# Kernel optimization log

Measured on AMD Instinct MI355X. Metric: run time of the kernel, lower is better.

Reference implementation:

```python
import jax, jax.numpy as jnp
import numpy as np

N_NODES = 50000
N_FEAT = 128
N_EDGES = 800000
HEADS1 = 4
HID1 = 64
HID2 = 128
N_CLASSES = 10
N_GRAPHS = 512
NEG_SLOPE_ATT = 0.2   # GATConv attention leaky relu
NEG_SLOPE_ACT = 0.01  # F.leaky_relu default between layers


def setup_inputs() -> dict:
    key = jax.random.key(0)
    ks = jax.random.split(key, 20)
    s = 0.05
    inp = {
        'x': jax.random.normal(ks[0], (N_NODES, N_FEAT), dtype=jnp.float32),
        'edge_index': jax.random.randint(ks[1], (2, N_EDGES), 0, N_NODES, dtype=jnp.int64),
        'edge_attr': jax.random.normal(ks[2], (N_EDGES, 8), dtype=jnp.float32),
        'batch': jnp.sort(jax.random.randint(ks[3], (N_NODES,), 0, N_GRAPHS, dtype=jnp.int64)),
        # conv1: F -> HID1, heads=4, concat
        'W1': jax.random.normal(ks[4], (N_FEAT, HEADS1 * HID1), dtype=jnp.float32) * s,
        'a_src1': jax.random.normal(ks[5], (HEADS1, HID1), dtype=jnp.float32) * s,
        'a_dst1': jax.random.normal(ks[6], (HEADS1, HID1), dtype=jnp.float32) * s,
        'b1': jnp.zeros((HEADS1 * HID1,), dtype=jnp.float32),
        # conv2: 4*HID1 -> HID2, heads=1
        'W2': jax.random.normal(ks[7], (HEADS1 * HID1, HID2), dtype=jnp.float32) * s,
        'a_src2': jax.random.normal(ks[8], (1, HID2), dtype=jnp.float32) * s,
        'a_dst2': jax.random.normal(ks[9], (1, HID2), dtype=jnp.float32) * s,
        'b2': jnp.zeros((HID2,), dtype=jnp.float32),
        # conv3: HID2 -> N_CLASSES, heads=1
        'W3': jax.random.normal(ks[10], (HID2, N_CLASSES), dtype=jnp.float32) * s,
        'a_src3': jax.random.normal(ks[11], (1, N_CLASSES), dtype=jnp.float32) * s,
        'a_dst3': jax.random.normal(ks[12], (1, N_CLASSES), dtype=jnp.float32) * s,
        'b3': jnp.zeros((N_CLASSES,), dtype=jnp.float32),
    }
    return inp


def gat_conv(x, src, dst, W, a_src, a_dst, b, n_nodes, heads, ch):
    """PyG GATConv (concat=True, add_self_loops already applied in src/dst)."""
    h = (x @ W).reshape(n_nodes, heads, ch)            # [N,H,C]
    al_s = (h * a_src).sum(-1)                          # [N,H]
    al_d = (h * a_dst).sum(-1)                          # [N,H]
    e = jax.nn.leaky_relu(al_s[src] + al_d[dst], NEG_SLOPE_ATT)  # [E,H]
    # segment softmax over incoming edges per destination node
    m = jax.ops.segment_max(e, dst, num_segments=n_nodes)
    ex = jnp.exp(e - m[dst])
    den = jax.ops.segment_sum(ex, dst, num_segments=n_nodes)
    alpha = ex / (den[dst] + 1e-16)                     # [E,H]
    out = jax.ops.segment_sum(h[src] * alpha[..., None], dst, num_segments=n_nodes)
    return out.reshape(n_nodes, heads * ch) + b


def reference(x, edge_index, edge_attr, batch,
              W1, a_src1, a_dst1, b1,
              W2, a_src2, a_dst2, b2,
              W3, a_src3, a_dst3, b3):
    # GATConv adds self-loops by default; edge_attr unused (edge_dim=None)
    loops = jnp.arange(N_NODES, dtype=edge_index.dtype)
    src = jnp.concatenate([edge_index[0], loops])
    dst = jnp.concatenate([edge_index[1], loops])

    h = gat_conv(x, src, dst, W1, a_src1, a_dst1, b1, N_NODES, HEADS1, HID1)
    h = jax.nn.leaky_relu(h, NEG_SLOPE_ACT)
    h = gat_conv(h, src, dst, W2, a_src2, a_dst2, b2, N_NODES, 1, HID2)
    h = jax.nn.leaky_relu(h, NEG_SLOPE_ACT)
    h = gat_conv(h, src, dst, W3, a_src3, a_dst3, b3, N_NODES, 1, N_CLASSES)

    pooled = jax.ops.segment_sum(h, batch, num_segments=N_GRAPHS)  # global_add_pool
    return jax.nn.log_softmax(pooled, axis=1), pooled
```

## Files before the change

kernel.cpp:

```cpp
#include <hip/hip_runtime.h>
#include <math.h>

#define NNODES 50000
#define MPAD   50048
#define NFEAT  128
#define NEDGE  800000
#define ETOT   (NEDGE + NNODES)
#define H1     4
#define O1     256
#define C2     128
#define C3     10
#define NGRAPH 512

#define NBKT   196
#define NBLK1  831
#define EPB    1024
#define SCM    (NBKT * NBLK1)
#define SCB    637

typedef __attribute__((ext_vector_type(8))) short short8;
typedef __attribute__((ext_vector_type(4))) float f32x4;
typedef __attribute__((ext_vector_type(2))) float f32x2;

__device__ __forceinline__ unsigned short f2b(float f) {
  unsigned int u = __float_as_uint(f);
  u += 0x7fffu + ((u >> 16) & 1u);
  return (unsigned short)(u >> 16);
}
__device__ __forceinline__ float b2f(unsigned short u) {
  return __uint_as_float(((unsigned int)u) << 16);
}
__device__ __forceinline__ float readlane_f(float v, int l) {
  return __uint_as_float((unsigned)__builtin_amdgcn_readlane(__float_as_uint(v), l));
}


__global__ void k_prep(const float* __restrict__ W1, const float* __restrict__ as1,
                       const float* __restrict__ ad1,
                       float* __restrict__ was, float* __restrict__ wad) {
  int tid = threadIdx.x;
  int h = tid >> 7, k = tid & 127;
  float s = 0.f, d = 0.f;
  for (int j = 0; j < 64; ++j) {
    float w = W1[(size_t)k * 256 + h * 64 + j];
    s += w * as1[h * 64 + j];
    d += w * ad1[h * 64 + j];
  }
  was[h * 128 + k] = s;
  wad[h * 128 + k] = d;
}

#define NB_CVT 12500

__global__ __launch_bounds__(256) void k_front(
    const int* __restrict__ src_e, const int* __restrict__ dst_e,
    int* __restrict__ hists,
    const float* __restrict__ X, unsigned short* __restrict__ Xb,
    const float* __restrict__ W1,
    const float* __restrict__ was, const float* __restrict__ wad,
    float* __restrict__ als, float* __restrict__ ald,
    unsigned short* __restrict__ W1p,
    const float* __restrict__ W2, unsigned short* __restrict__ W2p,
    const float* __restrict__ W3, unsigned short* __restrict__ W3p) {
  const int b = blockIdx.x;
  const int tid = threadIdx.x;
  if (b < NBLK1) {
    __shared__ int h[NBKT];
    if (tid < NBKT) h[tid] = 0;
    __syncthreads();
    const int base = b * EPB;
#pragma unroll
    for (int r = 0; r < 4; ++r) {
      int e = base + r * 256 + tid;
      if (e < ETOT) {
        int d = (e < NEDGE) ? dst_e[e] : (e - NEDGE);
        atomicAdd(&h[d >> 8], 1);
      }
    }
    __syncthreads();
    if (tid < NBKT) hists[tid * NBLK1 + b] = h[tid];
  } else if (b < NBLK1 + NB_CVT) {
    const int n = (b - NBLK1) * 4 + (tid >> 6);
    const int lane = tid & 63;
    const int k0 = lane * 2;
    float2 xv = *(const float2*)(X + (size_t)n * 128 + k0);
    ushort2 o; o.x = f2b(xv.x); o.y = f2b(xv.y);
    *(ushort2*)(Xb + (size_t)n * 128 + k0) = o;
    float s[4], d[4];
#pragma unroll
    for (int h = 0; h < 4; ++h) {
      float2 wsv = *(const float2*)(was + h * 128 + k0);
      float2 wdv = *(const float2*)(wad + h * 128 + k0);
      s[h] = xv.x * wsv.x + xv.y * wsv.y;
      d[h] = xv.x * wdv.x + xv.y * wdv.y;
    }
#pragma unroll
    for (int m = 1; m < 64; m <<= 1)
#pragma unroll
      for (int h = 0; h < 4; ++h) { s[h] += __shfl_xor(s[h], m); d[h] += __shfl_xor(d[h], m); }
    if (lane == 0) {
#pragma unroll
      for (int h = 0; h < 4; ++h) {
        als[(size_t)n * 4 + h] = s[h];
        ald[(size_t)n * 4 + h] = d[h];
      }
    }
  } else if (b < NBLK1 + NB_CVT + 128) {
    int idx = (b - NBLK1 - NB_CVT) * 256 + tid;
    int h = idx >> 13, r = idx & 8191;
    int j = r & 7, lane = (r >> 3) & 63, t = r >> 9;
    int ks = t & 3, nt = t >> 2;
    int k = ks * 32 + (lane >> 4) * 8 + j;
    int n = nt * 16 + (lane & 15);
    W1p[idx] = f2b(W1[(size_t)k * 256 + h * 64 + n]);
  } else if (b < NBLK1 + NB_CVT + 256) {
    int idx = (b - NBLK1 - NB_CVT - 128) * 256 + tid;
    int j = idx & 7, lane = (idx >> 3) & 63, t = idx >> 9;
    int ks = t % 8, nt = t / 8;
    int k = ks * 32 + (lane >> 4) * 8 + j;
    int n = nt * 16 + (lane & 15);
    W2p[idx] = f2b(W2[(size_t)k * C2 + n]);
  } else {
    int idx = (b - NBLK1 - NB_CVT - 256) * 256 + tid;
    int j = idx & 7, lane = (idx >> 3) & 63, t = idx >> 9;
    int ks = t & 3, nt = t >> 2;
    int k = ks * 32 + (lane >> 4) * 8 + j;
    int n = nt * 16 + (lane & 15);
    W3p[idx] = f2b((n < C3) ? W3[(size_t)k * C3 + n] : 0.f);
  }
}


__global__ __launch_bounds__(256) void k_scanA2(const int* __restrict__ a,
                                                int* __restrict__ bsum) {
  int idx = blockIdx.x * 256 + threadIdx.x;
  int v = (idx < SCM) ? a[idx] : 0;
#pragma unroll
  for (int m = 1; m < 64; m <<= 1) v += __shfl_xor(v, m);
  __shared__ int ws[4];
  int lane = threadIdx.x & 63, wid = threadIdx.x >> 6;
  if (lane == 0) ws[wid] = v;
  __syncthreads();
  if (threadIdx.x == 0) bsum[blockIdx.x] = ws[0] + ws[1] + ws[2] + ws[3];
}

__global__ __launch_bounds__(256) void k_scanMid(int* __restrict__ bsum) {
  __shared__ int ws[4];
  __shared__ int carry_s;
  const int tid = threadIdx.x, lane = tid & 63, wid = tid >> 6;
  if (tid == 0) carry_s = 0;
  __syncthreads();
  for (int base = 0; base < SCB; base += 256) {
    int j = base + tid;
    int v = (j < SCB) ? bsum[j] : 0;
    int s = v;
#pragma unroll
    for (int m = 1; m < 64; m <<= 1) {
      int t = __shfl_up(s, m);
      if (lane >= m) s += t;
    }
    if (lane == 63) ws[wid] = s;
    __syncthreads();
    int woff = 0;
#pragma unroll
    for (int k = 0; k < 4; ++k)
      if (k < wid) woff += ws[k];
    int c = carry_s;
    int tot = ws[0] + ws[1] + ws[2] + ws[3];
    if (j < SCB) bsum[j] = c + woff + s - v;
    __syncthreads();
    if (tid == 0) carry_s = c + tot;
    __syncthreads();
  }
}

__global__ __launch_bounds__(256) void k_scanB2(int* __restrict__ a,
                                                const int* __restrict__ bsum,
                                                int* __restrict__ cb) {
  const int b = blockIdx.x, tid = threadIdx.x;
  const int lane = tid & 63, wid = tid >> 6;
  __shared__ int ws[4];
  int idx = b * 256 + tid;
  int v = (idx < SCM) ? a[idx] : 0;
  int s = v;
#pragma unroll
  for (int m = 1; m < 64; m <<= 1) {
    int t = __shfl_up(s, m);
    if (lane >= m) s += t;
  }
  if (lane == 63) ws[wid] = s;
  __syncthreads();
  int woff = 0;
#pragma unroll
  for (int k = 0; k < 4; ++k)
    if (k < wid) woff += ws[k];
  int excl = bsum[b] + woff + s - v;
  if (idx < SCM) {
    a[idx] = excl;
    if (idx % NBLK1 == 0) cb[idx / NBLK1] = excl;
  }
  if (b == 0 && tid == 0) cb[NBKT] = ETOT;
}


__global__ __launch_bounds__(256) void k_part1(const int* __restrict__ src_e,
                                               const int* __restrict__ dst_e,
                                               const int* __restrict__ offs,
                                               unsigned* __restrict__ coarse) {
  __shared__ int cur[NBKT];
  const int b = blockIdx.x;
  const int tid = threadIdx.x;
  if (tid < NBKT) cur[tid] = offs[tid * NBLK1 + b];
  __syncthreads();
  const int base = b * EPB;
#pragma unroll
  for (int r = 0; r < 4; ++r) {
    int e = base + r * 256 + tid;
    if (e < ETOT) {
      int d, s;
      if (e < NEDGE) { d = dst_e[e]; s = src_e[e]; }
      else           { d = e - NEDGE; s = e - NEDGE; }
      int pos = atomicAdd(&cur[d >> 8], 1);
      coarse[pos] = ((unsigned)d << 16) | (unsigned)s;
    }
  }
}


__global__ __launch_bounds__(256) void k_bucket(const unsigned* __restrict__ coarse,
                                                const int* __restrict__ cb,
                                                int* __restrict__ rowptr,
                                                int* __restrict__ srcs) {
  const int b = blockIdx.x;
  const int tid = threadIdx.x;
  const int lane = tid & 63, wid = tid >> 6;
  const int lo = cb[b], hi = cb[b + 1];
  __shared__ int h[256];
  __shared__ int cur[256];
  __shared__ int ws[4];
  h[tid] = 0;
  __syncthreads();
  for (int i = lo + tid; i < hi; i += 256)
    atomicAdd(&h[(coarse[i] >> 16) & 255], 1);
  __syncthreads();
  int v = h[tid];
  int s = v;
#pragma unroll
  for (int m = 1; m < 64; m <<= 1) {
    int t = __shfl_up(s, m);
    if (lane >= m) s += t;
  }
  if (lane == 63) ws[wid] = s;
  __syncthreads();
  int woff = 0;
#pragma unroll
  for (int k = 0; k < 4; ++k)
    if (k < wid) woff += ws[k];
  int ex = woff + s - v;
  cur[tid] = lo + ex;
  int d = b * 256 + tid;
  if (d < NNODES) rowptr[d] = lo + ex;
  if (b == NBKT - 1 && tid == 0) rowptr[NNODES] = ETOT;
  __syncthreads();
  for (int i = lo + tid; i < hi; i += 256) {
    unsigned c = coarse[i];
    int pos = atomicAdd(&cur[(c >> 16) & 255], 1);
    srcs[pos] = (int)(c & 0xffffu);
  }
}


__global__ __launch_bounds__(512) void k_aggP(const int* __restrict__ rowptr,
                                              const int* __restrict__ srcs,
                                              const unsigned short* __restrict__ Xb,
                                              const float* __restrict__ als,
                                              const float* __restrict__ ald,
                                              unsigned short* __restrict__ P) {
  __shared__ float exs[8][16][4];
  const int wv = threadIdx.x >> 6;
  const int n = blockIdx.x * 8 + wv;
  const int lane = threadIdx.x & 63;
  const int r0 = rowptr[n], r1 = rowptr[n + 1];
  const int e_lane = lane & 15, hh = lane >> 4;
  const float aldv = ald[(size_t)n * 4 + hh];
  const int ch0 = lane * 2;
  f32x2 ah0 = {0.f, 0.f}, ah1 = {0.f, 0.f}, ah2 = {0.f, 0.f}, ah3 = {0.f, 0.f};
  float den = 0.f;
  for (int i0 = r0; i0 < r1; i0 += 16) {
    const int take = r1 - i0;
    int sidx = srcs[min(i0 + e_lane, r1 - 1)];
    float ev = als[(size_t)sidx * 4 + hh] + aldv;
    ev = (ev > 0.f) ? ev : 0.2f * ev;
    float exv = (e_lane < take) ? __expf(ev) : 0.f;
    den += exv;
    exs[wv][e_lane][hh] = exv;
    unsigned hv[16];
#pragma unroll
    for (int m = 0; m < 16; ++m) {
      int s = __builtin_amdgcn_readlane(sidx, m);
      hv[m] = *(const unsigned*)(Xb + (size_t)s * 128 + ch0);
    }
#pragma unroll
    for (int m = 0; m < 16; ++m) {
      f32x2 e01 = *(const f32x2*)(&exs[wv][m][0]);
      f32x2 e23 = *(const f32x2*)(&exs[wv][m][2]);
      f32x2 x2;
      x2.x = __uint_as_float(hv[m] << 16);
      x2.y = __uint_as_float(hv[m] & 0xffff0000u);
      asm("v_pk_fma_f32 %0, %1, %2, %0 op_sel:[0,0,0] op_sel_hi:[1,0,1]"
          : "+v"(ah0) : "v"(x2), "v"(e01));
      asm("v_pk_fma_f32 %0, %1, %2, %0 op_sel:[0,1,0] op_sel_hi:[1,1,1]"
          : "+v"(ah1) : "v"(x2), "v"(e01));
      asm("v_pk_fma_f32 %0, %1, %2, %0 op_sel:[0,0,0] op_sel_hi:[1,0,1]"
          : "+v"(ah2) : "v"(x2), "v"(e23));
      asm("v_pk_fma_f32 %0, %1, %2, %0 op_sel:[0,1,0] op_sel_hi:[1,1,1]"
          : "+v"(ah3) : "v"(x2), "v"(e23));
    }
  }
#pragma unroll
  for (int m = 1; m < 16; m <<= 1) den += __shfl_xor(den, m);
  float acc[4][2] = {{ah0.x, ah0.y}, {ah1.x, ah1.y}, {ah2.x, ah2.y}, {ah3.x, ah3.y}};
#pragma unroll
  for (int h = 0; h < 4; ++h) {
    float rd = 1.f / (readlane_f(den, h * 16) + 1e-16f);
    ushort2 o; o.x = f2b(acc[h][0] * rd); o.y = f2b(acc[h][1] * rd);
    *(ushort2*)(P + ((size_t)n * 4 + h) * 128 + ch0) = o;
  }
}


__global__ __launch_bounds__(256) void k_mmX(
    const unsigned short* __restrict__ P,
    const unsigned short* __restrict__ W1p, const float* __restrict__ b1,
    const unsigned short* __restrict__ W2p,
    const float* __restrict__ as2, const float* __restrict__ ad2,
    unsigned short* __restrict__ Hout,
    float* __restrict__ als, float* __restrict__ ald) {
  __shared__ unsigned short actl[64 * 256];
  const int wv = threadIdx.x >> 6, lane = threadIdx.x & 63;
  const int row16 = lane & 15;
  const int k0 = (lane >> 4) * 8;
  const int col = lane & 15;
  const int rb = (lane >> 4) * 4;

  const int nodebase = blockIdx.x * 64 + wv * 16;
#pragma unroll
  for (int h = 0; h < 4; ++h) {
    const unsigned short* Ph = P + ((size_t)(nodebase + row16) * 4 + h) * 128;
    f32x4 acc[4] = {};
#pragma unroll
    for (int ks = 0; ks < 4; ++ks) {
      short8 a = *(const short8*)(Ph + ks * 32 + k0);
      const short8* bp = (const short8*)(W1p + (size_t)h * 8192) + ks * 64 + lane;
#pragma unroll
      for (int nt = 0; nt < 4; ++nt) {
        short8 b = bp[nt * 256];
        acc[nt] = __builtin_amdgcn_mfma_f32_16x16x32_bf16(a, b, acc[nt], 0, 0, 0);
      }
    }
#pragma unroll
    for (int nt = 0; nt < 4; ++nt) {
      int ch = h * 64 + nt * 16 + col;
      float bb = b1[ch];
#pragma unroll
      for (int j = 0; j < 4; ++j) {
        int row = wv * 16 + rb + j;
        float v = acc[nt][j] + bb;
        v = (v > 0.f) ? v : 0.01f * v;
        unsigned byte = (unsigned)(row * 512 + ch * 2) ^ (unsigned)((row & 7) << 4);
        *(unsigned short*)((char*)actl + byte) = f2b(v);
      }
    }
  }
  __syncthreads();

  const int arow = wv * 16 + row16;
  f32x4 acc2[8] = {};
#pragma unroll
  for (int ks = 0; ks < 8; ++ks) {
    unsigned byte = (unsigned)(arow * 512 + (ks * 32 + k0) * 2) ^
                    (unsigned)((arow & 7) << 4);
    short8 a = *(const short8*)((const char*)actl + byte);
    const short8* bp = (const short8*)W2p + ks * 64 + lane;
#pragma unroll
    for (int nt = 0; nt < 8; ++nt) {
      short8 b = bp[(size_t)nt * 512];
      acc2[nt] = __builtin_amdgcn_mfma_f32_16x16x32_bf16(a, b, acc2[nt], 0, 0, 0);
    }
  }
  const int rbase = blockIdx.x * 64 + wv * 16 + rb;
  float av[8], dv[8];
#pragma unroll
  for (int nt = 0; nt < 8; ++nt) {
    int ch = nt * 16 + col;
    av[nt] = as2[ch];
    dv[nt] = ad2[ch];
#pragma unroll
    for (int j = 0; j < 4; ++j)
      Hout[(size_t)(rbase + j) * C2 + ch] = f2b(acc2[nt][j]);
  }
  float sa[4] = {0.f, 0.f, 0.f, 0.f}, da[4] = {0.f, 0.f, 0.f, 0.f};
#pragma unroll
  for (int nt = 0; nt < 8; ++nt)
#pragma unroll
    for (int j = 0; j < 4; ++j) {
      sa[j] += acc2[nt][j] * av[nt];
      da[j] += acc2[nt][j] * dv[nt];
    }
#pragma unroll
  for (int mask = 1; mask < 16; mask <<= 1)
#pragma unroll
    for (int j = 0; j < 4; ++j) {
      sa[j] += __shfl_xor(sa[j], mask);
      da[j] += __shfl_xor(da[j], mask);
    }
  if (col == 0) {
#pragma unroll
    for (int j = 0; j < 4; ++j) {
      als[rbase + j] = sa[j];
      ald[rbase + j] = da[j];
    }
  }
}


__global__ __launch_bounds__(512) void k_agg2(const int* __restrict__ rowptr,
                                              const int* __restrict__ srcs,
                                              const unsigned short* __restrict__ Hm,
                                              const float* __restrict__ als,
                                              const float* __restrict__ ald,
                                              const float* __restrict__ bias,
                                              const unsigned short* __restrict__ W3p,
                                              const float* __restrict__ as3,
                                              const float* __restrict__ ad3,
                                              unsigned short* __restrict__ H3b,
                                              float* __restrict__ als3,
                                              float* __restrict__ ald3) {
  __shared__ float exs2[8][16];
  __shared__ unsigned short Xl[8][128];
  const int wv = threadIdx.x >> 6;
  const int n = blockIdx.x * 8 + wv;
  const int lane = threadIdx.x & 63;
  const int r0 = rowptr[n], r1 = rowptr[n + 1];
  const int e_lane = lane & 15;
  const int ch0 = lane * 2;
  const float aldm = ald[n];
  f32x2 accP0 = {0.f, 0.f}, accP1 = {0.f, 0.f};
  float den = 0.f;
  for (int i0 = r0; i0 < r1; i0 += 16) {
    const int take = r1 - i0;
    int sidx = srcs[min(i0 + e_lane, r1 - 1)];
    float ev = als[sidx] + aldm;
    ev = (ev > 0.f) ? ev : 0.2f * ev;
    float exv = (lane < 16 && e_lane < take) ? __expf(ev) : 0.f;
    den += exv;
    if (lane < 16) exs2[wv][lane] = exv;
    unsigned hv[16];
#pragma unroll
    for (int m = 0; m < 16; ++m) {
      int s = __builtin_amdgcn_readlane(sidx, m);
      hv[m] = *(const unsigned*)(Hm + (size_t)s * C2 + ch0);
    }
#pragma unroll
    for (int m = 0; m < 16; m += 2) {
      f32x2 ep = *(const f32x2*)(&exs2[wv][m]);
      f32x2 xa, xb;
      xa.x = __uint_as_float(hv[m] << 16);
      xa.y = __uint_as_float(hv[m + 1] << 16);
      xb.x = __uint_as_float(hv[m] & 0xffff0000u);
      xb.y = __uint_as_float(hv[m + 1] & 0xffff0000u);
      asm("v_pk_fma_f32 %0, %1, %2, %0" : "+v"(accP0) : "v"(ep), "v"(xa));
      asm("v_pk_fma_f32 %0, %1, %2, %0" : "+v"(accP1) : "v"(ep), "v"(xb));
    }
  }
#pragma unroll
  for (int mask = 1; mask < 64; mask <<= 1) den += __shfl_xor(den, mask);
  float rden = 1.f / (den + 1e-16f);
  float v0 = (accP0.x + accP0.y) * rden + bias[ch0];
  float v1 = (accP1.x + accP1.y) * rden + bias[ch0 + 1];
  v0 = (v0 > 0.f) ? v0 : 0.01f * v0;
  v1 = (v1 > 0.f) ? v1 : 0.01f * v1;
  ushort2 o; o.x = f2b(v0); o.y = f2b(v1);
  *(ushort2*)(&Xl[wv][ch0]) = o;
  __syncthreads();

  if (wv == 0) {
    const int row = lane & 15;
    const int k0 = (lane >> 4) * 8;
    const int col = lane & 15;
    f32x4 acc2 = {};
#pragma unroll
    for (int ks = 0; ks < 4; ++ks) {
      short8 a{};
      if (row < 8) a = *(const short8*)(&Xl[row][ks * 32 + k0]);
      short8 b = *((const short8*)W3p + ks * 64 + lane);
      acc2 = __builtin_amdgcn_mfma_f32_16x16x32_bf16(a, b, acc2, 0, 0, 0);
    }
    const float av = (col < C3) ? as3[col] : 0.f;
    const float dv = (col < C3) ? ad3[col] : 0.f;
    const int rb = (lane >> 4) * 4;
#pragma unroll
    for (int j = 0; j < 4; ++j) {
      float hv = acc2[j];
      float sa = hv * av, da = hv * dv;
#pragma unroll
      for (int mask = 1; mask < 16; mask <<= 1) {
        sa += __shfl_xor(sa, mask);
        da += __shfl_xor(da, mask);
      }
      int r = rb + j;
      if (r < 8) {
        int node = blockIdx.x * 8 + r;
        H3b[(size_t)node * 16 + col] = f2b(hv);
        if (col == 0) { als3[node] = sa; ald3[node] = da; }
      }
    }
  }
}


__global__ __launch_bounds__(512) void k_agg3(const int* __restrict__ rowptr,
                                              const int* __restrict__ srcs,
                                              const unsigned short* __restrict__ Hm,
                                              const float* __restrict__ als,
                                              const float* __restrict__ ald,
                                              const float* __restrict__ bias,
                                              float* __restrict__ pooled,
                                              const int* __restrict__ batch) {
  __shared__ int   sid_s[8][4][16];
  __shared__ float exv_s[8][4][16];
  const int wv = threadIdx.x >> 6;
  const int lane = threadIdx.x & 63;
  const int g = lane >> 4, el = lane & 15;
  const int n = blockIdx.x * 32 + wv * 4 + g;
  const bool valid = n < NNODES;
  int r0 = 0, r1 = 0;
  float aldm = 0.f;
  if (valid) { r0 = rowptr[n]; r1 = rowptr[n + 1]; aldm = ald[n]; }
  float acc = 0.f, den = 0.f;
  for (int i0 = r0; i0 < r1; i0 += 16) {
    const int take = r1 - i0;
    int sidx = srcs[min(i0 + el, r1 - 1)];
    float ev = als[sidx] + aldm;
    ev = (ev > 0.f) ? ev : 0.2f * ev;
    float exv = (el < take) ? __expf(ev) : 0.f;
    den += exv;
    sid_s[wv][g][el] = sidx;
    exv_s[wv][g][el] = exv;
#pragma unroll
    for (int m = 0; m < 16; ++m) {
      int s = sid_s[wv][g][m];
      float ex = exv_s[wv][g][m];
      acc += ex * b2f(Hm[(size_t)s * 16 + el]);
    }
  }
#pragma unroll
  for (int mask = 1; mask < 16; mask <<= 1) den += __shfl_xor(den, mask);
  if (valid && el < C3) {
    float val = acc / (den + 1e-16f) + bias[el];
    atomicAdd(&pooled[(size_t)batch[n] * C3 + el], val);
  }
}


__global__ void k_lsm(const float* __restrict__ pooled, float* __restrict__ dout) {
  int g = blockIdx.x * 256 + threadIdx.x;
  if (g >= NGRAPH) return;
  float v[C3];
  float mx = -1e30f;
#pragma unroll
  for (int c = 0; c < C3; ++c) { v[c] = pooled[g * C3 + c]; mx = fmaxf(mx, v[c]); }
  float ssum = 0.f;
#pragma unroll
  for (int c = 0; c < C3; ++c) ssum += __expf(v[c] - mx);
  float lse = mx + __logf(ssum);
#pragma unroll
  for (int c = 0; c < C3; ++c) {
    dout[g * C3 + c] = v[c] - lse;
    dout[NGRAPH * C3 + g * C3 + c] = v[c];
  }
}


extern "C" void kernel_launch(void* const* d_in, const int* in_sizes, int n_in,
                              void* d_out, int out_size, void* d_ws, size_t ws_size,
                              hipStream_t stream) {
  (void)in_sizes; (void)n_in; (void)out_size; (void)ws_size;
  const float* x     = (const float*)d_in[0];
  const int*   eix   = (const int*)d_in[1];
  const int*   batch = (const int*)d_in[3];
  const float* W1 = (const float*)d_in[4];
  const float* as1 = (const float*)d_in[5];
  const float* ad1 = (const float*)d_in[6];
  const float* b1 = (const float*)d_in[7];
  const float* W2 = (const float*)d_in[8];
  const float* as2 = (const float*)d_in[9];
  const float* ad2 = (const float*)d_in[10];
  const float* b2 = (const float*)d_in[11];
  const float* W3 = (const float*)d_in[12];
  const float* as3 = (const float*)d_in[13];
  const float* ad3 = (const float*)d_in[14];
  const float* b3 = (const float*)d_in[15];
  const int* src_e = eix;
  const int* dst_e = eix + NEDGE;

  char* ws = (char*)d_ws;
  size_t off = 0;
  auto carve = [&](size_t bytes) -> char* {
    char* p = ws + off;
    off += (bytes + 511) & ~(size_t)511;
    return p;
  };
  int* hists  = (int*)carve((size_t)SCM * 4);
  int* bsum   = (int*)carve((size_t)SCB * 4);
  int* cb     = (int*)carve((size_t)(NBKT + 1) * 4);
  unsigned* coarse = (unsigned*)carve((size_t)ETOT * 4);
  int* rowptr = (int*)carve((size_t)(NNODES + 1) * 4);
  int* srcs   = (int*)carve((size_t)ETOT * 4);
  float* als  = (float*)carve((size_t)MPAD * H1 * 4);
  float* ald  = (float*)carve((size_t)MPAD * H1 * 4);
  float* als3 = (float*)carve((size_t)MPAD * 4);
  float* ald3 = (float*)carve((size_t)MPAD * 4);
  float* was  = (float*)carve((size_t)512 * 4);
  float* wad  = (float*)carve((size_t)512 * 4);
  unsigned short* Xb  = (unsigned short*)carve((size_t)MPAD * 128 * 2);
  unsigned short* P   = (unsigned short*)carve((size_t)MPAD * 512 * 2);
  unsigned short* Hb  = (unsigned short*)carve((size_t)MPAD * 128 * 2);
  unsigned short* H3b = (unsigned short*)carve((size_t)MPAD * 16 * 2);
  float* pooled = (float*)carve((size_t)NGRAPH * C3 * 4);
  unsigned short* W1p = (unsigned short*)carve((size_t)4 * 8192 * 2);
  unsigned short* W2p = (unsigned short*)carve((size_t)O1 * C2 * 2);
  unsigned short* W3p = (unsigned short*)carve((size_t)C2 * 16 * 2);

  hipMemsetAsync(pooled, 0, (size_t)NGRAPH * C3 * 4, stream);

  k_prep<<<1, 512, 0, stream>>>(W1, as1, ad1, was, wad);
  k_front<<<NBLK1 + NB_CVT + 264, 256, 0, stream>>>(
      src_e, dst_e, hists, x, Xb, W1, was, wad, als, ald, W1p, W2, W2p, W3, W3p);
  k_scanA2<<<SCB, 256, 0, stream>>>(hists, bsum);
  k_scanMid<<<1, 256, 0, stream>>>(bsum);
  k_scanB2<<<SCB, 256, 0, stream>>>(hists, bsum, cb);
  k_part1<<<NBLK1, 256, 0, stream>>>(src_e, dst_e, hists, coarse);
  k_bucket<<<NBKT, 256, 0, stream>>>(coarse, cb, rowptr, srcs);

  const int GB = MPAD / 64;
  const int NB8 = NNODES / 8;
  const int NB32 = (NNODES + 31) / 32;

  k_aggP<<<NB8, 512, 0, stream>>>(rowptr, srcs, Xb, als, ald, P);
  k_mmX<<<GB, 256, 0, stream>>>(P, W1p, b1, W2p, as2, ad2, Hb, als, ald);

  k_agg2<<<NB8, 512, 0, stream>>>(rowptr, srcs, Hb, als, ald, b2,
                                  W3p, as3, ad3, H3b, als3, ald3);

  k_agg3<<<NB32, 512, 0, stream>>>(rowptr, srcs, H3b, als3, ald3, b3, pooled, batch);

  k_lsm<<<(NGRAPH + 255) / 256, 256, 0, stream>>>(pooled, (float*)d_out);
}
```

Baseline: 222.0 us.

## Drop scanMid and memset launches, compute layer-3 projection per-wave without block sync

The zeroing of pooled moves into k_prep, replacing a separate memset. The single-block k_scanMid is removed, and each k_scanB2 block now sums the preceding block totals itself, which removes one serialized launch at the cost of redundant reads of up to 637 values per block. In k_agg2, the block-wide __syncthreads followed by a single-wave MFMA over 8 rows is replaced with each wave running its own MFMA on its row after only an LDS waitcnt. This removes the barrier and the serial tail, but each wave now uses only one row of the 16-row MFMA.

```diff
diff --git a/kernel.cpp b/kernel.cpp
--- a/kernel.cpp
+++ b/kernel.cpp
@@ -37,8 +37,10 @@
 
 __global__ void k_prep(const float* __restrict__ W1, const float* __restrict__ as1,
                        const float* __restrict__ ad1,
-                       float* __restrict__ was, float* __restrict__ wad) {
+                       float* __restrict__ was, float* __restrict__ wad,
+                       float* __restrict__ pooled) {
   int tid = threadIdx.x;
+  for (int i = tid; i < NGRAPH * C3; i += 512) pooled[i] = 0.f;
   int h = tid >> 7, k = tid & 127;
   float s = 0.f, d = 0.f;
   for (int j = 0; j < 64; ++j) {
@@ -144,42 +146,23 @@
   if (threadIdx.x == 0) bsum[blockIdx.x] = ws[0] + ws[1] + ws[2] + ws[3];
 }
 
-__global__ __launch_bounds__(256) void k_scanMid(int* __restrict__ bsum) {
-  __shared__ int ws[4];
-  __shared__ int carry_s;
-  const int tid = threadIdx.x, lane = tid & 63, wid = tid >> 6;
-  if (tid == 0) carry_s = 0;
-  __syncthreads();
-  for (int base = 0; base < SCB; base += 256) {
-    int j = base + tid;
-    int v = (j < SCB) ? bsum[j] : 0;
-    int s = v;
-#pragma unroll
-    for (int m = 1; m < 64; m <<= 1) {
-      int t = __shfl_up(s, m);
-      if (lane >= m) s += t;
-    }
-    if (lane == 63) ws[wid] = s;
-    __syncthreads();
-    int woff = 0;
-#pragma unroll
-    for (int k = 0; k < 4; ++k)
-      if (k < wid) woff += ws[k];
-    int c = carry_s;
-    int tot = ws[0] + ws[1] + ws[2] + ws[3];
-    if (j < SCB) bsum[j] = c + woff + s - v;
-    __syncthreads();
-    if (tid == 0) carry_s = c + tot;
-    __syncthreads();
-  }
-}
-
 __global__ __launch_bounds__(256) void k_scanB2(int* __restrict__ a,
                                                 const int* __restrict__ bsum,
                                                 int* __restrict__ cb) {
   const int b = blockIdx.x, tid = threadIdx.x;
   const int lane = tid & 63, wid = tid >> 6;
   __shared__ int ws[4];
+  __shared__ int ws2[4];
+  int part = 0;
+  for (int i0 = 0; i0 < SCB; i0 += 256) {
+    int i = i0 + tid;
+    if (i < b) part += bsum[i];
+  }
+#pragma unroll
+  for (int m = 1; m < 64; m <<= 1) part += __shfl_xor(part, m);
+  if (lane == 0) ws2[wid] = part;
+  __syncthreads();
+  const int boff = ws2[0] + ws2[1] + ws2[2] + ws2[3];
   int idx = b * 256 + tid;
   int v = (idx < SCM) ? a[idx] : 0;
   int s = v;
@@ -194,7 +177,7 @@
 #pragma unroll
   for (int k = 0; k < 4; ++k)
     if (k < wid) woff += ws[k];
-  int excl = bsum[b] + woff + s - v;
+  int excl = boff + woff + s - v;
   if (idx < SCM) {
     a[idx] = excl;
     if (idx % NBLK1 == 0) cb[idx / NBLK1] = excl;
@@ -482,40 +465,28 @@
   v1 = (v1 > 0.f) ? v1 : 0.01f * v1;
   ushort2 o; o.x = f2b(v0); o.y = f2b(v1);
   *(ushort2*)(&Xl[wv][ch0]) = o;
-  __syncthreads();
-
-  if (wv == 0) {
-    const int row = lane & 15;
-    const int k0 = (lane >> 4) * 8;
-    const int col = lane & 15;
-    f32x4 acc2 = {};
-#pragma unroll
-    for (int ks = 0; ks < 4; ++ks) {
-      short8 a{};
-      if (row < 8) a = *(const short8*)(&Xl[row][ks * 32 + k0]);
-      short8 b = *((const short8*)W3p + ks * 64 + lane);
-      acc2 = __builtin_amdgcn_mfma_f32_16x16x32_bf16(a, b, acc2, 0, 0, 0);
-    }
-    const float av = (col < C3) ? as3[col] : 0.f;
-    const float dv = (col < C3) ? ad3[col] : 0.f;
-    const int rb = (lane >> 4) * 4;
-#pragma unroll
-    for (int j = 0; j < 4; ++j) {
-      float hv = acc2[j];
-      float sa = hv * av, da = hv * dv;
-#pragma unroll
-      for (int mask = 1; mask < 16; mask <<= 1) {
-        sa += __shfl_xor(sa, mask);
-        da += __shfl_xor(da, mask);
-      }
-      int r = rb + j;
-      if (r < 8) {
-        int node = blockIdx.x * 8 + r;
-        H3b[(size_t)node * 16 + col] = f2b(hv);
-        if (col == 0) { als3[node] = sa; ald3[node] = da; }
-      }
-    }
-  }
+  asm volatile("s_waitcnt lgkmcnt(0)" ::: "memory");
+
+  const int k0 = (lane >> 4) * 8;
+  const int col = lane & 15;
+  f32x4 acc2 = {};
+#pragma unroll
+  for (int ks = 0; ks < 4; ++ks) {
+    short8 a = *(const short8*)(&Xl[wv][ks * 32 + k0]);
+    short8 b = *((const short8*)W3p + ks * 64 + lane);
+    acc2 = __builtin_amdgcn_mfma_f32_16x16x32_bf16(a, b, acc2, 0, 0, 0);
+  }
+  float hv = acc2[0];
+  const float av = (col < C3) ? as3[col] : 0.f;
+  const float dv = (col < C3) ? ad3[col] : 0.f;
+  float sa = hv * av, da = hv * dv;
+#pragma unroll
+  for (int mask = 1; mask < 16; mask <<= 1) {
+    sa += __shfl_xor(sa, mask);
+    da += __shfl_xor(da, mask);
+  }
+  if (lane < 16) H3b[(size_t)n * 16 + col] = f2b(hv);
+  if (lane == 0) { als3[n] = sa; ald3[n] = da; }
 }
 
 
@@ -632,13 +603,10 @@
   unsigned short* W2p = (unsigned short*)carve((size_t)O1 * C2 * 2);
   unsigned short* W3p = (unsigned short*)carve((size_t)C2 * 16 * 2);
 
-  hipMemsetAsync(pooled, 0, (size_t)NGRAPH * C3 * 4, stream);
-
-  k_prep<<<1, 512, 0, stream>>>(W1, as1, ad1, was, wad);
+  k_prep<<<1, 512, 0, stream>>>(W1, as1, ad1, was, wad, pooled);
   k_front<<<NBLK1 + NB_CVT + 264, 256, 0, stream>>>(
       src_e, dst_e, hists, x, Xb, W1, was, wad, als, ald, W1p, W2, W2p, W3, W3p);
   k_scanA2<<<SCB, 256, 0, stream>>>(hists, bsum);
-  k_scanMid<<<1, 256, 0, stream>>>(bsum);
   k_scanB2<<<SCB, 256, 0, stream>>>(hists, bsum, cb);
   k_part1<<<NBLK1, 256, 0, stream>>>(src_e, dst_e, hists, coarse);
   k_bucket<<<NBKT, 256, 0, stream>>>(coarse, cb, rowptr, srcs);
```

Result: faster. 213.1 us (-4.0%).
